# Performance work log

Measured on AMD Instinct MI355X. Metric: run time of the kernel, lower is better.

The kernel has to match this reference:

```python
import jax, jax.numpy as jnp
import numpy as np

L_MAX = 2048
D_E = 768
D_V = 64
H = 12
D_MLP = 3072
VOCAB = 32000
N_LAYERS = 4


def setup_inputs() -> dict:
    key = jax.random.key(0)
    ks = iter(jax.random.split(key, 32))
    s = 0.02
    def nrm(shape):
        return jax.random.normal(next(ks), shape, dtype=jnp.float32) * s
    return {
        "x": jax.random.randint(next(ks), (L_MAX,), 0, VOCAB, dtype=jnp.int32),
        "word_embed": nrm((VOCAB, D_E)),
        "pos_embed": nrm((L_MAX, D_E)),
        "Wq": nrm((N_LAYERS, H, D_E, D_E)), "bq": nrm((N_LAYERS, H, D_E)),
        "Wk": nrm((N_LAYERS, H, D_E, D_E)), "bk": nrm((N_LAYERS, H, D_E)),
        "Wv": nrm((N_LAYERS, H, D_E, D_V)), "bv": nrm((N_LAYERS, H, D_V)),
        "Wo": nrm((N_LAYERS, H * D_V, D_E)), "bo": nrm((N_LAYERS, D_E)),
        "g1": nrm((N_LAYERS, D_E)), "be1": nrm((N_LAYERS, D_E)),
        "g2": nrm((N_LAYERS, D_E)), "be2": nrm((N_LAYERS, D_E)),
        "W1": nrm((N_LAYERS, D_E, D_MLP)), "bm1": nrm((N_LAYERS, D_MLP)),
        "W2": nrm((N_LAYERS, D_MLP, D_E)), "bm2": nrm((N_LAYERS, D_E)),
        "gf": nrm((D_E,)), "bef": nrm((D_E,)),
        "Wu": nrm((D_E, VOCAB)), "bu": nrm((VOCAB,)),
    }


def _layernorm(x, gamma, beta):
    # Original applies LayerNormalization row by row: scalar mean/std per row,
    # shared gamma/beta of shape (d_e,). Vectorized over rows.
    mean = jnp.mean(x, axis=-1, keepdims=True)
    std = jnp.std(x, axis=-1, keepdims=True)
    std = jnp.where(std == 0, jnp.ones_like(std), std)
    return gamma * ((x - mean) / std) + beta


def _mha(xn, Wq, bq, Wk, bk, Wv, bv, Wo, bo):
    # All heads computed; d_attn == d_e in this model.
    q = jnp.einsum('ld,hde->hle', xn, Wq) + bq[:, None, :]
    k = jnp.einsum('ld,hde->hle', xn, Wk) + bk[:, None, :]
    v = jnp.einsum('ld,hdv->hlv', xn, Wv) + bv[:, None, :]
    scores = jnp.einsum('hle,hme->hlm', q, k) / np.float32(np.sqrt(D_E))
    attn = jnp.einsum('hlm,hmv->hlv', jax.nn.softmax(scores, axis=-1), v)  # (H, l, d_v)
    # Faithful to the original overlapping writes y.at[:, idx:idx+d_v].set(...):
    # later heads overwrite earlier ones, so head idx<H-1 survives only in column idx
    # (its output column 0), head H-1 occupies [H-1, H-1+d_v), rest stays zero.
    l = xn.shape[0]
    y = jnp.zeros((l, H * D_V), xn.dtype)
    y = y.at[:, :H - 1].set(attn[:H - 1, :, 0].T)
    y = y.at[:, H - 1:H - 1 + D_V].set(attn[H - 1])
    return y @ Wo + bo


def _forward(x, word_embed, pos_embed, Wq, bq, Wk, bk, Wv, bv, Wo, bo,
             g1, be1, g2, be2, W1, bm1, W2, bm2, gf, bef, Wu, bu):
    Y = word_embed[x] + pos_embed[:x.shape[0]]  # (l, d_e)
    for i in range(N_LAYERS):
        xn = _layernorm(Y, g1[i], be1[i])
        # original: x.at[:, :].add(x + mha) == 2*x + mha
        Y = 2.0 * Y + _mha(xn, Wq[i], bq[i], Wk[i], bk[i], Wv[i], bv[i], Wo[i], bo[i])
        zn = _layernorm(Y, g2[i], be2[i])
        # x + act_layer(zn), act_layer(zn) = zn + mlp2(gelu(mlp1(zn)))
        Y = Y + zn + jax.nn.gelu(zn @ W1[i] + bm1[i]) @ W2[i] + bm2[i]
    Yn = _layernorm(Y, gf, bef)
    return jax.nn.softmax(Yn @ Wu + bu, axis=-1)


def reference(x, word_embed, pos_embed, Wq, bq, Wk, bk, Wv, bv, Wo, bo,
              g1, be1, g2, be2, W1, bm1, W2, bm2, gf, bef, Wu, bu):
    return _forward(x, word_embed, pos_embed, Wq, bq, Wk, bk, Wv, bv, Wo, bo,
                    g1, be1, g2, be2, W1, bm1, W2, bm2, gf, bef, Wu, bu)
```

## Files before the change

### kernel.cpp

```cpp
#include <hip/hip_runtime.h>

#define L_SEQ 2048
#define DE 768
#define DV 64
#define NH 12
#define DMLP 3072
#define NVOCAB 32000
#define NLAYERS 4

typedef float f32x4 __attribute__((ext_vector_type(4)));
typedef __bf16 bf16x8 __attribute__((ext_vector_type(8)));

__device__ __forceinline__ unsigned short f2bf(float f) {
  union { float f; unsigned int u; } x; x.f = f;
  unsigned int r = x.u + 0x7fffu + ((x.u >> 16) & 1u);
  return (unsigned short)(r >> 16);
}
__device__ __forceinline__ float bf2f(unsigned short u) {
  union { unsigned int u; float f; } x; x.u = ((unsigned int)u) << 16;
  return x.f;
}
__device__ __forceinline__ float gelu_f(float x) {
  float x3 = x * x * x;
  return 0.5f * x * (1.f + tanhf(0.7978845608028654f * (x + 0.044715f * x3)));
}

__global__ void embed_kernel(const int* __restrict__ x, const float* __restrict__ we,
                             const float* __restrict__ pe, float* __restrict__ Y) {
  int l = blockIdx.x;
  int id = x[l];
  for (int c = threadIdx.x; c < DE; c += 256)
    Y[(long)l * DE + c] = we[(long)id * DE + c] + pe[(long)l * DE + c];
}

__global__ void layernorm_kernel(const float* __restrict__ X, const float* __restrict__ g,
                                 const float* __restrict__ be, float* __restrict__ outf,
                                 unsigned short* __restrict__ outb) {
  __shared__ float red1[4], red2[4];
  int row = blockIdx.x;
  const float* xr = X + (long)row * DE;
  int tid = threadIdx.x;
  float xv[3];
  float s = 0.f, sq = 0.f;
#pragma unroll
  for (int j = 0; j < 3; j++) {
    float v = xr[tid + 256 * j];
    xv[j] = v; s += v; sq += v * v;
  }
#pragma unroll
  for (int o = 32; o; o >>= 1) { s += __shfl_down(s, o, 64); sq += __shfl_down(sq, o, 64); }
  int wave = tid >> 6, lane = tid & 63;
  if (lane == 0) { red1[wave] = s; red2[wave] = sq; }
  __syncthreads();
  s = red1[0] + red1[1] + red1[2] + red1[3];
  sq = red2[0] + red2[1] + red2[2] + red2[3];
  float mean = s * (1.f / DE);
  float var = fmaxf(sq * (1.f / DE) - mean * mean, 0.f);
  float sd = sqrtf(var);
  if (sd == 0.f) sd = 1.f;
  float inv = 1.f / sd;
#pragma unroll
  for (int j = 0; j < 3; j++) {
    int c = tid + 256 * j;
    float o = g[c] * ((xv[j] - mean) * inv) + be[c];
    if (outf) outf[(long)row * DE + c] = o;
    outb[(long)row * DE + c] = f2bf(o);
  }
}

__global__ void transpose_cvt(const float* __restrict__ in, long sInZ,
                              unsigned short* __restrict__ out, long sOutZ, int R, int C) {
  __shared__ float tile[32][33];
  const float* inz = in + (long)blockIdx.z * sInZ;
  unsigned short* outz = out + (long)blockIdx.z * sOutZ;
  int c0 = blockIdx.x * 32, r0 = blockIdx.y * 32;
  int tx = threadIdx.x, ty = threadIdx.y;
#pragma unroll
  for (int j = 0; j < 32; j += 8) {
    int r = r0 + ty + j, c = c0 + tx;
    tile[ty + j][tx] = (r < R && c < C) ? inz[(long)r * C + c] : 0.f;
  }
  __syncthreads();
#pragma unroll
  for (int j = 0; j < 32; j += 8) {
    int orow = c0 + ty + j, oc = r0 + tx;
    if (orow < C && oc < R) outz[(long)orow * R + oc] = f2bf(tile[tx][ty + j]);
  }
}

__global__ void transpose_bf16(const unsigned short* __restrict__ in, long sInZ,
                               unsigned short* __restrict__ out, long sOutZ, int R, int C) {
  __shared__ unsigned short tile[32][33];
  const unsigned short* inz = in + (long)blockIdx.z * sInZ;
  unsigned short* outz = out + (long)blockIdx.z * sOutZ;
  int c0 = blockIdx.x * 32, r0 = blockIdx.y * 32;
  int tx = threadIdx.x, ty = threadIdx.y;
#pragma unroll
  for (int j = 0; j < 32; j += 8) {
    int r = r0 + ty + j, c = c0 + tx;
    tile[ty + j][tx] = (r < R && c < C) ? inz[(long)r * C + c] : (unsigned short)0;
  }
  __syncthreads();
#pragma unroll
  for (int j = 0; j < 32; j += 8) {
    int orow = c0 + ty + j, oc = r0 + tx;
    if (orow < C && oc < R) outz[(long)orow * R + oc] = tile[tx][ty + j];
  }
}

__global__ void softmax_rows_bf16(unsigned short* __restrict__ S) {
  __shared__ float redm[4], reds[4];
  long row = blockIdx.x;
  unsigned short* s = S + row * (long)L_SEQ;
  int tid = threadIdx.x;
  float v[8];
  float m = -1e30f;
#pragma unroll
  for (int j = 0; j < 8; j++) { v[j] = bf2f(s[tid + 256 * j]); m = fmaxf(m, v[j]); }
#pragma unroll
  for (int o = 1; o < 64; o <<= 1) m = fmaxf(m, __shfl_xor(m, o, 64));
  int wave = tid >> 6, lane = tid & 63;
  if (lane == 0) redm[wave] = m;
  __syncthreads();
  m = fmaxf(fmaxf(redm[0], redm[1]), fmaxf(redm[2], redm[3]));
  float sum = 0.f;
#pragma unroll
  for (int j = 0; j < 8; j++) { v[j] = __expf(v[j] - m); sum += v[j]; }
#pragma unroll
  for (int o = 1; o < 64; o <<= 1) sum += __shfl_xor(sum, o, 64);
  if (lane == 0) reds[wave] = sum;
  __syncthreads();
  sum = reds[0] + reds[1] + reds[2] + reds[3];
  float inv = 1.f / sum;
#pragma unroll
  for (int j = 0; j < 8; j++) s[tid + 256 * j] = f2bf(v[j] * inv);
}

__global__ void softmax_rows_f32(float* __restrict__ S, int cols) {
  __shared__ float redm[4], reds[4];
  long row = blockIdx.x;
  float* s = S + row * (long)cols;
  int tid = threadIdx.x;
  float m = -1e30f, sum = 0.f;
  for (int c = tid; c < cols; c += 256) {
    float v = s[c];
    if (v > m) { sum = sum * __expf(m - v) + 1.f; m = v; }
    else sum += __expf(v - m);
  }
#pragma unroll
  for (int o = 1; o < 64; o <<= 1) {
    float m2 = __shfl_xor(m, o, 64), s2 = __shfl_xor(sum, o, 64);
    float M = fmaxf(m, m2);
    sum = sum * __expf(m - M) + s2 * __expf(m2 - M);
    m = M;
  }
  int wave = tid >> 6, lane = tid & 63;
  if (lane == 0) { redm[wave] = m; reds[wave] = sum; }
  __syncthreads();
  float M = fmaxf(fmaxf(redm[0], redm[1]), fmaxf(redm[2], redm[3]));
  float ssum = reds[0] * __expf(redm[0] - M) + reds[1] * __expf(redm[1] - M) +
               reds[2] * __expf(redm[2] - M) + reds[3] * __expf(redm[3] - M);
  float inv = 1.f / ssum;
  for (int c = tid; c < cols; c += 256) s[c] = __expf(s[c] - M) * inv;
}

__global__ void assemble_y(const unsigned short* __restrict__ attn, unsigned short* __restrict__ y) {
  int l = blockIdx.x;
  for (int c = threadIdx.x; c < DE; c += 256) {
    unsigned short v = 0;
    if (c < NH - 1) v = attn[(long)c * L_SEQ * DV + (long)l * DV + 0];
    else if (c < NH - 1 + DV) v = attn[(long)(NH - 1) * L_SEQ * DV + (long)l * DV + (c - (NH - 1))];
    y[(long)l * DE + c] = v;
  }
}

template <bool OUT_BF16, bool GELU_ACT>
__global__ __launch_bounds__(256) void gemm_bf16(
    const unsigned short* __restrict__ A, long sAz,
    const unsigned short* __restrict__ B, long sBz,
    void* __restrict__ Cv, long sCz,
    const float* __restrict__ bias, long sBiasz,
    const float* __restrict__ res1, float alpha,
    const float* __restrict__ res2,
    float scale, int M, int N, int K) {
  __shared__ unsigned short As[128 * 32];
  __shared__ unsigned short Bs[128 * 32];
  const int tid = threadIdx.x;
  const int z = blockIdx.z;
  const unsigned short* Az = A + (long)z * sAz;
  const unsigned short* Bz = B + (long)z * sBz;
  const float* biasz = bias ? (bias + (long)z * sBiasz) : nullptr;
  const int n0 = blockIdx.x * 128;
  const int m0 = blockIdx.y * 128;
  const int wave = tid >> 6;
  const int lane = tid & 63;
  const int wm = (wave >> 1) * 64;
  const int wn = (wave & 1) * 64;
  const int l16 = lane & 15;
  const int quad = lane >> 4;
  const int r1 = tid >> 2;
  const int c1 = (tid & 3) * 8;

  f32x4 zero4 = {0.f, 0.f, 0.f, 0.f};
  f32x4 acc[4][4];
#pragma unroll
  for (int i = 0; i < 4; i++)
#pragma unroll
    for (int j = 0; j < 4; j++) acc[i][j] = zero4;

  const unsigned short* Ap0 = Az + (long)(m0 + r1) * K + c1;
  const unsigned short* Ap1 = Az + (long)(m0 + r1 + 64) * K + c1;
  const int brow0 = n0 + r1, brow1 = n0 + r1 + 64;
  const unsigned short* Bp0 = Bz + (long)brow0 * K + c1;
  const unsigned short* Bp1 = Bz + (long)brow1 * K + c1;
  const bool bok0 = (brow0 < N), bok1 = (brow1 < N);

  for (int kk = 0; kk < K; kk += 32) {
    uint4 a0 = *(const uint4*)(Ap0 + kk);
    uint4 a1 = *(const uint4*)(Ap1 + kk);
    uint4 b0; b0.x = b0.y = b0.z = b0.w = 0u;
    uint4 b1 = b0;
    if (bok0) b0 = *(const uint4*)(Bp0 + kk);
    if (bok1) b1 = *(const uint4*)(Bp1 + kk);
    __syncthreads();
    *(uint4*)(&As[r1 * 32 + c1]) = a0;
    *(uint4*)(&As[(r1 + 64) * 32 + c1]) = a1;
    *(uint4*)(&Bs[r1 * 32 + c1]) = b0;
    *(uint4*)(&Bs[(r1 + 64) * 32 + c1]) = b1;
    __syncthreads();
    bf16x8 af[4], bfv[4];
#pragma unroll
    for (int t = 0; t < 4; t++) {
      af[t]  = *(const bf16x8*)(&As[(wm + t * 16 + l16) * 32 + quad * 8]);
      bfv[t] = *(const bf16x8*)(&Bs[(wn + t * 16 + l16) * 32 + quad * 8]);
    }
#pragma unroll
    for (int mt = 0; mt < 4; mt++)
#pragma unroll
      for (int nt = 0; nt < 4; nt++)
        acc[mt][nt] = __builtin_amdgcn_mfma_f32_16x16x32_bf16(af[mt], bfv[nt], acc[mt][nt], 0, 0, 0);
  }

#pragma unroll
  for (int nt = 0; nt < 4; nt++) {
    const int col = n0 + wn + nt * 16 + l16;
    if (col >= N) continue;
    const float bval = biasz ? biasz[col] : 0.f;
#pragma unroll
    for (int mt = 0; mt < 4; mt++) {
#pragma unroll
      for (int r = 0; r < 4; r++) {
        const int row = m0 + wm + mt * 16 + quad * 4 + r;
        float v = acc[mt][nt][r] * scale + bval;
        if (GELU_ACT) v = gelu_f(v);
        const long idx = (long)row * N + col;
        if (res1) v += alpha * res1[idx];
        if (res2) v += res2[idx];
        if (OUT_BF16) ((unsigned short*)Cv)[(long)z * sCz + idx] = f2bf(v);
        else ((float*)Cv)[(long)z * sCz + idx] = v;
      }
    }
  }
}

extern "C" void kernel_launch(void* const* d_in, const int* in_sizes, int n_in,
                              void* d_out, int out_size, void* d_ws, size_t ws_size,
                              hipStream_t stream) {
  const int* x        = (const int*)d_in[0];
  const float* we     = (const float*)d_in[1];
  const float* pe     = (const float*)d_in[2];
  const float* Wq     = (const float*)d_in[3];
  const float* bq     = (const float*)d_in[4];
  const float* Wk     = (const float*)d_in[5];
  const float* bk     = (const float*)d_in[6];
  const float* Wv     = (const float*)d_in[7];
  const float* bv     = (const float*)d_in[8];
  const float* Wo     = (const float*)d_in[9];
  const float* bo     = (const float*)d_in[10];
  const float* g1     = (const float*)d_in[11];
  const float* be1    = (const float*)d_in[12];
  const float* g2     = (const float*)d_in[13];
  const float* be2    = (const float*)d_in[14];
  const float* W1     = (const float*)d_in[15];
  const float* bm1    = (const float*)d_in[16];
  const float* W2     = (const float*)d_in[17];
  const float* bm2    = (const float*)d_in[18];
  const float* gf     = (const float*)d_in[19];
  const float* bef    = (const float*)d_in[20];
  const float* Wu     = (const float*)d_in[21];
  const float* bu     = (const float*)d_in[22];
  float* out          = (float*)d_out;
  const int L = L_SEQ;

  char* base = (char*)d_ws;
  size_t off = 0;
  auto alloc = [&](size_t b) -> void* {
    void* p = base + off;
    off = (off + b + 255) & ~(size_t)255;
    return p;
  };
  float* Yf             = (float*)alloc((size_t)L * DE * 4);
  float* normf          = (float*)alloc((size_t)L * DE * 4);
  unsigned short* normb = (unsigned short*)alloc((size_t)L * DE * 2);
  unsigned short* Qb    = (unsigned short*)alloc((size_t)NH * L * DE * 2);
  unsigned short* Kb    = (unsigned short*)alloc((size_t)NH * L * DE * 2);
  unsigned short* Vb    = (unsigned short*)alloc((size_t)NH * L * DV * 2);
  unsigned short* Vtb   = (unsigned short*)alloc((size_t)NH * DV * L * 2);
  unsigned short* attnb = (unsigned short*)alloc((size_t)NH * L * DV * 2);
  unsigned short* yb    = (unsigned short*)alloc((size_t)L * DE * 2);
  unsigned short* hb    = (unsigned short*)alloc((size_t)L * DMLP * 2);
  unsigned short* wqt   = (unsigned short*)alloc((size_t)NH * DE * DE * 2);
  unsigned short* wkt   = (unsigned short*)alloc((size_t)NH * DE * DE * 2);
  unsigned short* wvt   = (unsigned short*)alloc((size_t)NH * DV * DE * 2);
  unsigned short* wot   = (unsigned short*)alloc((size_t)DE * DE * 2);
  unsigned short* w1t   = (unsigned short*)alloc((size_t)DMLP * DE * 2);
  unsigned short* w2t   = (unsigned short*)alloc((size_t)DE * DMLP * 2);
  unsigned short* scores= (unsigned short*)alloc((size_t)NH * L * L * 2);
  unsigned short* wut   = scores;
  (void)ws_size; (void)in_sizes; (void)n_in; (void)out_size;

  const dim3 tb(256);
  const dim3 tt(32, 8);
  const float inv_sqrt_de = 0.03608439182435161f;

  embed_kernel<<<dim3(L), tb, 0, stream>>>(x, we, pe, Yf);

  for (int i = 0; i < NLAYERS; i++) {
    transpose_cvt<<<dim3(24, 24, NH), tt, 0, stream>>>(Wq + (long)i * NH * DE * DE, (long)DE * DE, wqt, (long)DE * DE, DE, DE);
    transpose_cvt<<<dim3(24, 24, NH), tt, 0, stream>>>(Wk + (long)i * NH * DE * DE, (long)DE * DE, wkt, (long)DE * DE, DE, DE);
    transpose_cvt<<<dim3(2, 24, NH), tt, 0, stream>>>(Wv + (long)i * NH * DE * DV, (long)DE * DV, wvt, (long)DV * DE, DE, DV);
    transpose_cvt<<<dim3(24, 24, 1), tt, 0, stream>>>(Wo + (long)i * DE * DE, 0, wot, 0, DE, DE);
    transpose_cvt<<<dim3(96, 24, 1), tt, 0, stream>>>(W1 + (long)i * DE * DMLP, 0, w1t, 0, DE, DMLP);
    transpose_cvt<<<dim3(24, 96, 1), tt, 0, stream>>>(W2 + (long)i * DMLP * DE, 0, w2t, 0, DMLP, DE);

    layernorm_kernel<<<dim3(L), tb, 0, stream>>>(Yf, g1 + (long)i * DE, be1 + (long)i * DE, nullptr, normb);

    gemm_bf16<true, false><<<dim3(6, 16, NH), tb, 0, stream>>>(
        normb, 0L, wqt, (long)DE * DE, Qb, (long)L * DE,
        bq + (long)i * NH * DE, (long)DE, nullptr, 0.f, nullptr, 1.f, L, DE, DE);
    gemm_bf16<true, false><<<dim3(6, 16, NH), tb, 0, stream>>>(
        normb, 0L, wkt, (long)DE * DE, Kb, (long)L * DE,
        bk + (long)i * NH * DE, (long)DE, nullptr, 0.f, nullptr, 1.f, L, DE, DE);
    gemm_bf16<true, false><<<dim3(1, 16, NH), tb, 0, stream>>>(
        normb, 0L, wvt, (long)DV * DE, Vb, (long)L * DV,
        bv + (long)i * NH * DV, (long)DV, nullptr, 0.f, nullptr, 1.f, L, DV, DE);

    gemm_bf16<true, false><<<dim3(16, 16, NH), tb, 0, stream>>>(
        Qb, (long)L * DE, Kb, (long)L * DE, scores, (long)L * L,
        nullptr, 0L, nullptr, 0.f, nullptr, inv_sqrt_de, L, L, DE);

    softmax_rows_bf16<<<dim3(NH * L), tb, 0, stream>>>(scores);

    transpose_bf16<<<dim3(2, 64, NH), tt, 0, stream>>>(Vb, (long)L * DV, Vtb, (long)DV * L, L, DV);

    gemm_bf16<true, false><<<dim3(1, 16, NH), tb, 0, stream>>>(
        scores, (long)L * L, Vtb, (long)DV * L, attnb, (long)L * DV,
        nullptr, 0L, nullptr, 0.f, nullptr, 1.f, L, DV, L);

    assemble_y<<<dim3(L), tb, 0, stream>>>(attnb, yb);

    gemm_bf16<false, false><<<dim3(6, 16, 1), tb, 0, stream>>>(
        yb, 0L, wot, 0L, Yf, 0L,
        bo + (long)i * DE, 0L, Yf, 2.f, nullptr, 1.f, L, DE, DE);

    layernorm_kernel<<<dim3(L), tb, 0, stream>>>(Yf, g2 + (long)i * DE, be2 + (long)i * DE, normf, normb);

    gemm_bf16<true, true><<<dim3(24, 16, 1), tb, 0, stream>>>(
        normb, 0L, w1t, 0L, hb, 0L,
        bm1 + (long)i * DMLP, 0L, nullptr, 0.f, nullptr, 1.f, L, DMLP, DE);

    gemm_bf16<false, false><<<dim3(6, 16, 1), tb, 0, stream>>>(
        hb, 0L, w2t, 0L, Yf, 0L,
        bm2 + (long)i * DE, 0L, Yf, 1.f, normf, 1.f, L, DE, DMLP);
  }

  layernorm_kernel<<<dim3(L), tb, 0, stream>>>(Yf, gf, bef, nullptr, normb);

  transpose_cvt<<<dim3(1000, 24, 1), tt, 0, stream>>>(Wu, 0, wut, 0, DE, NVOCAB);

  gemm_bf16<false, false><<<dim3(250, 16, 1), tb, 0, stream>>>(
      normb, 0L, wut, 0L, out, 0L,
      bu, 0L, nullptr, 0.f, nullptr, 1.f, L, NVOCAB, DE);

  softmax_rows_f32<<<dim3(L), tb, 0, stream>>>(out, NVOCAB);
}
```

Measured before the change: 3.168 ms.

## Load GEMM tiles directly to LDS and vectorize softmax row kernels

The GEMM main loop now uses global_load_lds to copy A and B tiles straight from global memory into shared memory, skipping the register round trip. Out-of-range B rows are clamped to the last valid row instead of being zero-filled. Both softmax kernels switch to 16-byte vectorized loads and stores, and the fp32 online softmax takes its max over four values at a time. The direct-to-LDS path still has no double buffering, so load latency stays exposed between the two barriers. The clamped B rows only feed output columns that are never written, so results are unaffected. It also relies on the per-wave LDS layout matching the As/Bs indexing the MFMA fragment reads expect.

```diff
diff --git a/kernel.cpp b/kernel.cpp
--- a/kernel.cpp
+++ b/kernel.cpp
@@ -23,6 +23,12 @@
 __device__ __forceinline__ float gelu_f(float x) {
   float x3 = x * x * x;
   return 0.5f * x * (1.f + tanhf(0.7978845608028654f * (x + 0.044715f * x3)));
+}
+
+__device__ __forceinline__ void gld_lds16(const void* g, void* lds) {
+  __builtin_amdgcn_global_load_lds(
+      (__attribute__((address_space(1))) void*)g,
+      (__attribute__((address_space(3))) void*)lds, 16, 0, 0);
 }
 
 __global__ void embed_kernel(const int* __restrict__ x, const float* __restrict__ we,
@@ -113,10 +119,12 @@
   long row = blockIdx.x;
   unsigned short* s = S + row * (long)L_SEQ;
   int tid = threadIdx.x;
+  union { uint4 u; unsigned short us[8]; } pk;
+  pk.u = *(const uint4*)(s + tid * 8);
   float v[8];
   float m = -1e30f;
 #pragma unroll
-  for (int j = 0; j < 8; j++) { v[j] = bf2f(s[tid + 256 * j]); m = fmaxf(m, v[j]); }
+  for (int j = 0; j < 8; j++) { v[j] = bf2f(pk.us[j]); m = fmaxf(m, v[j]); }
 #pragma unroll
   for (int o = 1; o < 64; o <<= 1) m = fmaxf(m, __shfl_xor(m, o, 64));
   int wave = tid >> 6, lane = tid & 63;
@@ -133,19 +141,22 @@
   sum = reds[0] + reds[1] + reds[2] + reds[3];
   float inv = 1.f / sum;
 #pragma unroll
-  for (int j = 0; j < 8; j++) s[tid + 256 * j] = f2bf(v[j] * inv);
+  for (int j = 0; j < 8; j++) pk.us[j] = f2bf(v[j] * inv);
+  *(uint4*)(s + tid * 8) = pk.u;
 }
 
 __global__ void softmax_rows_f32(float* __restrict__ S, int cols) {
   __shared__ float redm[4], reds[4];
   long row = blockIdx.x;
-  float* s = S + row * (long)cols;
+  f32x4* s4 = (f32x4*)(S + row * (long)cols);
+  const int n4 = cols >> 2;
   int tid = threadIdx.x;
   float m = -1e30f, sum = 0.f;
-  for (int c = tid; c < cols; c += 256) {
-    float v = s[c];
-    if (v > m) { sum = sum * __expf(m - v) + 1.f; m = v; }
-    else sum += __expf(v - m);
+  for (int c = tid; c < n4; c += 256) {
+    f32x4 v = s4[c];
+    float mc = fmaxf(fmaxf(v[0], v[1]), fmaxf(v[2], v[3]));
+    if (mc > m) { sum *= __expf(m - mc); m = mc; }
+    sum += __expf(v[0] - m) + __expf(v[1] - m) + __expf(v[2] - m) + __expf(v[3] - m);
   }
 #pragma unroll
   for (int o = 1; o < 64; o <<= 1) {
@@ -161,7 +172,14 @@
   float ssum = reds[0] * __expf(redm[0] - M) + reds[1] * __expf(redm[1] - M) +
                reds[2] * __expf(redm[2] - M) + reds[3] * __expf(redm[3] - M);
   float inv = 1.f / ssum;
-  for (int c = tid; c < cols; c += 256) s[c] = __expf(s[c] - M) * inv;
+  for (int c = tid; c < n4; c += 256) {
+    f32x4 v = s4[c];
+    v[0] = __expf(v[0] - M) * inv;
+    v[1] = __expf(v[1] - M) * inv;
+    v[2] = __expf(v[2] - M) * inv;
+    v[3] = __expf(v[3] - M) * inv;
+    s4[c] = v;
+  }
 }
 
 __global__ void assemble_y(const unsigned short* __restrict__ attn, unsigned short* __restrict__ y) {
@@ -200,6 +218,7 @@
   const int quad = lane >> 4;
   const int r1 = tid >> 2;
   const int c1 = (tid & 3) * 8;
+  const int wbase = wave * 512;
 
   f32x4 zero4 = {0.f, 0.f, 0.f, 0.f};
   f32x4 acc[4][4];
@@ -211,22 +230,17 @@
   const unsigned short* Ap0 = Az + (long)(m0 + r1) * K + c1;
   const unsigned short* Ap1 = Az + (long)(m0 + r1 + 64) * K + c1;
   const int brow0 = n0 + r1, brow1 = n0 + r1 + 64;
-  const unsigned short* Bp0 = Bz + (long)brow0 * K + c1;
-  const unsigned short* Bp1 = Bz + (long)brow1 * K + c1;
-  const bool bok0 = (brow0 < N), bok1 = (brow1 < N);
+  const int brow0c = brow0 < N ? brow0 : N - 1;
+  const int brow1c = brow1 < N ? brow1 : N - 1;
+  const unsigned short* Bp0 = Bz + (long)brow0c * K + c1;
+  const unsigned short* Bp1 = Bz + (long)brow1c * K + c1;
 
   for (int kk = 0; kk < K; kk += 32) {
-    uint4 a0 = *(const uint4*)(Ap0 + kk);
-    uint4 a1 = *(const uint4*)(Ap1 + kk);
-    uint4 b0; b0.x = b0.y = b0.z = b0.w = 0u;
-    uint4 b1 = b0;
-    if (bok0) b0 = *(const uint4*)(Bp0 + kk);
-    if (bok1) b1 = *(const uint4*)(Bp1 + kk);
     __syncthreads();
-    *(uint4*)(&As[r1 * 32 + c1]) = a0;
-    *(uint4*)(&As[(r1 + 64) * 32 + c1]) = a1;
-    *(uint4*)(&Bs[r1 * 32 + c1]) = b0;
-    *(uint4*)(&Bs[(r1 + 64) * 32 + c1]) = b1;
+    gld_lds16(Ap0 + kk, As + wbase);
+    gld_lds16(Ap1 + kk, As + 2048 + wbase);
+    gld_lds16(Bp0 + kk, Bs + wbase);
+    gld_lds16(Bp1 + kk, Bs + 2048 + wbase);
     __syncthreads();
     bf16x8 af[4], bfv[4];
 #pragma unroll
```

Result: no change. 3.157 ms (-0.3%).
